# Kernel optimization log

Hardware: AMD Instinct MI355X
Metric: run time of the kernel (lower is better)

## Reference

```python
import jax, jax.numpy as jnp
import numpy as np

N = 100_000   # nodes
IN = 256      # input feature size
H = 128       # hidden dim
OUT = 16      # output classes
R = 5         # relations
E = 100_000   # edges per relation
B = 2         # bases


def setup_inputs() -> dict:
    key = jax.random.key(0)
    ks = jax.random.split(key, 10)
    return {
        "x": jax.random.normal(ks[0], (N, IN), jnp.float32),
        "src": jax.random.randint(ks[1], (R, E), 0, N, dtype=jnp.int32),
        "dst": jax.random.randint(ks[2], (R, E), 0, N, dtype=jnp.int32),
        "w_embed": jax.random.normal(ks[3], (IN, H), jnp.float32) / np.sqrt(IN).astype(np.float32),
        "b_embed": jnp.zeros((H,), jnp.float32),
        "basis1": jax.random.normal(ks[4], (B, H, H), jnp.float32) / np.sqrt(H).astype(np.float32),
        "coef1": jax.random.normal(ks[5], (R, B), jnp.float32),
        "bias1": jnp.zeros((H,), jnp.float32),
        "basis2": jax.random.normal(ks[6], (B, H, OUT), jnp.float32) / np.sqrt(H).astype(np.float32),
        "coef2": jax.random.normal(ks[7], (R, B), jnp.float32),
        "bias2": jnp.zeros((OUT,), jnp.float32),
    }


def _rgcn_layer(h, src, dst, basis, coef, bias):
    # basis decomposition: W_r = sum_b coef[r,b] * V_b  -> [R, in, out]
    W = jnp.einsum('rb,bio->rio', coef, basis)

    def per_rel(s, d, w):
        msg = h[s] @ w                                        # [E, out] gather + GEMM
        agg = jax.ops.segment_sum(msg, d, num_segments=N)     # [N, out] scatter-add
        deg = jax.ops.segment_sum(jnp.ones((E,), h.dtype), d, num_segments=N)
        return agg / jnp.maximum(deg, 1.0)[:, None]           # fn.mean per relation

    out = jax.vmap(per_rel)(src, dst, W).sum(axis=0)          # 'sum' cross-relation reduce
    return out + bias


def reference(x, src, dst, w_embed, b_embed, basis1, coef1, bias1, basis2, coef2, bias2):
    h = x @ w_embed + b_embed                                 # EmbeddingLayer (Linear per ntype)
    h = jax.nn.relu(_rgcn_layer(h, src, dst, basis1, coef1, bias1))  # hidden RGCN layer, relu
    return _rgcn_layer(h, src, dst, basis2, coef2, bias2)     # output layer, no activation
```

## Files before the change

kernel.cpp:

```cpp
#include <hip/hip_runtime.h>
#include <hip/hip_bf16.h>
#include <cstddef>

namespace {

constexpr int N = 100000;
constexpr int IN = 256;
constexpr int H = 128;
constexpr int OUT = 16;
constexpr int R = 5;
constexpr int E = 100000;
constexpr int RE = R * E;
constexpr int NB = (N + 255) / 256;

using short8 = __attribute__((ext_vector_type(8))) short;
using f32x4 = __attribute__((ext_vector_type(4))) float;

__device__ __forceinline__ float b2f(unsigned int u16) {
  union { unsigned int i; float f; } v;
  v.i = u16 << 16;
  return v.f;
}
__device__ __forceinline__ unsigned short f2b(float f) {
  union { float f; unsigned int u; } v;
  v.f = f;
  unsigned int r = v.u + 0x7fffu + ((v.u >> 16) & 1u);
  return (unsigned short)(r >> 16);
}

__global__ void deg_count(const int* __restrict__ dst, float* __restrict__ deg,
                          int* __restrict__ degtot) {
  int i = blockIdx.x * 256 + threadIdx.x;
  if (i < RE) {
    int d = dst[i];
    atomicAdd(&deg[(i / E) * N + d], 1.0f);
    atomicAdd(&degtot[d], 1);
  }
}

__global__ void inv_deg_k(float* __restrict__ deg) {
  int i = blockIdx.x * 256 + threadIdx.x;
  if (i < R * N) deg[i] = 1.0f / fmaxf(deg[i], 1.0f);
}

__global__ void scan_blk(const int* __restrict__ in, int* __restrict__ part,
                         int* __restrict__ bsum, int n) {
  __shared__ int tmp[256];
  int tid = threadIdx.x;
  int gid = blockIdx.x * 256 + tid;
  int v = (gid < n) ? in[gid] : 0;
  tmp[tid] = v;
  __syncthreads();
  for (int o = 1; o < 256; o <<= 1) {
    int t = (tid >= o) ? tmp[tid - o] : 0;
    __syncthreads();
    tmp[tid] += t;
    __syncthreads();
  }
  if (gid < n) part[gid] = tmp[tid] - v;
  if (tid == 255) bsum[blockIdx.x] = tmp[255];
}

__global__ void scan_top(const int* __restrict__ bsum, int* __restrict__ bscan, int nb) {
  __shared__ int tmp[512];
  int tid = threadIdx.x;
  int v = (tid < nb) ? bsum[tid] : 0;
  tmp[tid] = v;
  __syncthreads();
  for (int o = 1; o < 512; o <<= 1) {
    int t = (tid >= o) ? tmp[tid - o] : 0;
    __syncthreads();
    tmp[tid] += t;
    __syncthreads();
  }
  if (tid < nb) bscan[tid] = tmp[tid] - v;
}

__global__ void scan_add(int* __restrict__ part, const int* __restrict__ bscan, int n) {
  int gid = blockIdx.x * 256 + threadIdx.x;
  if (gid < n) part[gid] += bscan[gid >> 8];
}

__global__ void fill_csr(const int* __restrict__ src, const int* __restrict__ dst,
                         const float* __restrict__ coef1, const float* __restrict__ coef2,
                         const float* __restrict__ invdeg, const int* __restrict__ off,
                         int* __restrict__ cursor, int* __restrict__ esrc,
                         float2* __restrict__ ecA, float2* __restrict__ ecB) {
  int i = blockIdx.x * 256 + threadIdx.x;
  if (i >= RE) return;
  int r = i / E;
  int d = dst[i];
  int slot = off[d] + atomicAdd(&cursor[d], 1);
  float id = invdeg[r * N + d];
  esrc[slot] = src[i];
  ecA[slot] = make_float2(coef1[2 * r] * id, coef1[2 * r + 1] * id);
  ecB[slot] = make_float2(coef2[2 * r] * id, coef2[2 * r + 1] * id);
}

__global__ void pack_w(const float* __restrict__ W, unsigned short* __restrict__ wp,
                       int NOUT, int total) {
  int i = blockIdx.x * 256 + threadIdx.x;
  if (i >= total) return;
  int ii = i & 7;
  int lane = (i >> 3) & 63;
  int fb = i >> 9;
  int NCT = NOUT >> 4;
  int kc = fb / NCT, ct = fb - kc * NCT;
  int k = kc * 32 + ((lane >> 4) << 3) + ii;
  int col = (ct << 4) + (lane & 15);
  wp[i] = f2b(W[(size_t)k * NOUT + col]);
}

__global__ void pack_b2(const float* __restrict__ basis2, unsigned short* __restrict__ wp) {
  int i = blockIdx.x * 256 + threadIdx.x;
  if (i >= 128 * 32) return;
  int ii = i & 7;
  int lane = (i >> 3) & 63;
  int fb = i >> 9;
  int kc = fb >> 1, ct = fb & 1;
  int k = kc * 32 + ((lane >> 4) << 3) + ii;
  wp[i] = f2b(basis2[((size_t)ct * 128 + k) * 16 + (lane & 15)]);
}

__global__ __launch_bounds__(256) void gemm_embed(
    const float* __restrict__ x, const unsigned short* __restrict__ wpack,
    const float* __restrict__ bias, unsigned short* __restrict__ C) {
  const int tid = threadIdx.x;
  const int lane = tid & 63;
  const int wave = (blockIdx.x * 256 + tid) >> 6;
  const int base = wave * 32;
  if (base >= N) return;
  const int r = lane & 15, g = lane >> 4;
  const short8* wfrag = (const short8*)wpack;

  f32x4 acc[2][8];
#pragma unroll
  for (int t = 0; t < 2; ++t)
#pragma unroll
    for (int ct = 0; ct < 8; ++ct) acc[t][ct] = (f32x4){0.f, 0.f, 0.f, 0.f};

  const float* a0 = x + (size_t)(base + r) * IN + g * 8;
  const float* a1 = a0 + (size_t)16 * IN;

#pragma unroll
  for (int kc = 0; kc < 8; ++kc) {
    float4 v0 = *(const float4*)(a0 + kc * 32);
    float4 v1 = *(const float4*)(a0 + kc * 32 + 4);
    float4 v2 = *(const float4*)(a1 + kc * 32);
    float4 v3 = *(const float4*)(a1 + kc * 32 + 4);
    short8 af0, af1;
    af0[0] = (short)f2b(v0.x); af0[1] = (short)f2b(v0.y);
    af0[2] = (short)f2b(v0.z); af0[3] = (short)f2b(v0.w);
    af0[4] = (short)f2b(v1.x); af0[5] = (short)f2b(v1.y);
    af0[6] = (short)f2b(v1.z); af0[7] = (short)f2b(v1.w);
    af1[0] = (short)f2b(v2.x); af1[1] = (short)f2b(v2.y);
    af1[2] = (short)f2b(v2.z); af1[3] = (short)f2b(v2.w);
    af1[4] = (short)f2b(v3.x); af1[5] = (short)f2b(v3.y);
    af1[6] = (short)f2b(v3.z); af1[7] = (short)f2b(v3.w);
#pragma unroll
    for (int ct = 0; ct < 8; ++ct) {
      short8 bf = wfrag[(kc * 8 + ct) * 64 + lane];
      acc[0][ct] = __builtin_amdgcn_mfma_f32_16x16x32_bf16(af0, bf, acc[0][ct], 0, 0, 0);
      acc[1][ct] = __builtin_amdgcn_mfma_f32_16x16x32_bf16(af1, bf, acc[1][ct], 0, 0, 0);
    }
  }

#pragma unroll
  for (int t = 0; t < 2; ++t)
#pragma unroll
    for (int ct = 0; ct < 8; ++ct) {
      int col = ct * 16 + r;
      float bs = bias[col];
#pragma unroll
      for (int i = 0; i < 4; ++i)
        C[(size_t)(base + t * 16 + g * 4 + i) * H + col] = f2b(acc[t][ct][i] + bs);
    }
}

__global__ __launch_bounds__(256) void gemm_fused(
    const unsigned short* __restrict__ u, const unsigned short* __restrict__ wp1,
    const float* __restrict__ bias1, const unsigned short* __restrict__ wp2,
    unsigned short* __restrict__ q) {
  constexpr int LP2 = 132;
  __shared__ unsigned short hl[4][32][LP2];
  const int tid = threadIdx.x;
  const int lane = tid & 63;
  const int wv = tid >> 6;
  const int wave = (blockIdx.x * 256 + tid) >> 6;
  const int base = wave * 32;
  if (base >= N) return;
  const int r = lane & 15, g = lane >> 4;
  const short8* wf1 = (const short8*)wp1;
  const short8* wf2 = (const short8*)wp2;

  f32x4 acc[2][8];
#pragma unroll
  for (int t = 0; t < 2; ++t)
#pragma unroll
    for (int ct = 0; ct < 8; ++ct) acc[t][ct] = (f32x4){0.f, 0.f, 0.f, 0.f};

  const unsigned short* a0 = u + (size_t)(base + r) * 256 + g * 8;
  const unsigned short* a1 = a0 + (size_t)16 * 256;

#pragma unroll
  for (int kc = 0; kc < 8; ++kc) {
    short8 af0 = *(const short8*)(a0 + kc * 32);
    short8 af1 = *(const short8*)(a1 + kc * 32);
#pragma unroll
    for (int ct = 0; ct < 8; ++ct) {
      short8 bf = wf1[(kc * 8 + ct) * 64 + lane];
      acc[0][ct] = __builtin_amdgcn_mfma_f32_16x16x32_bf16(af0, bf, acc[0][ct], 0, 0, 0);
      acc[1][ct] = __builtin_amdgcn_mfma_f32_16x16x32_bf16(af1, bf, acc[1][ct], 0, 0, 0);
    }
  }

#pragma unroll
  for (int t = 0; t < 2; ++t)
#pragma unroll
    for (int ct = 0; ct < 8; ++ct) {
      int col = ct * 16 + r;
      float bs = bias1[col];
#pragma unroll
      for (int i = 0; i < 4; ++i)
        hl[wv][t * 16 + g * 4 + i][col] = f2b(fmaxf(acc[t][ct][i] + bs, 0.f));
    }

  asm volatile("s_waitcnt lgkmcnt(0)" ::: "memory");
  __builtin_amdgcn_sched_barrier(0);

  f32x4 acc2[2][2];
#pragma unroll
  for (int t = 0; t < 2; ++t)
#pragma unroll
    for (int ct = 0; ct < 2; ++ct) acc2[t][ct] = (f32x4){0.f, 0.f, 0.f, 0.f};

#pragma unroll
  for (int kc = 0; kc < 4; ++kc) {
    short8 af0 = *(const short8*)&hl[wv][r][kc * 32 + g * 8];
    short8 af1 = *(const short8*)&hl[wv][16 + r][kc * 32 + g * 8];
#pragma unroll
    for (int ct = 0; ct < 2; ++ct) {
      short8 bf = wf2[(kc * 2 + ct) * 64 + lane];
      acc2[0][ct] = __builtin_amdgcn_mfma_f32_16x16x32_bf16(af0, bf, acc2[0][ct], 0, 0, 0);
      acc2[1][ct] = __builtin_amdgcn_mfma_f32_16x16x32_bf16(af1, bf, acc2[1][ct], 0, 0, 0);
    }
  }

#pragma unroll
  for (int t = 0; t < 2; ++t)
#pragma unroll
    for (int ct = 0; ct < 2; ++ct) {
      int col = ct * 16 + r;
#pragma unroll
      for (int i = 0; i < 4; ++i)
        q[(size_t)(base + t * 16 + g * 4 + i) * 32 + col] = f2b(acc2[t][ct][i]);
    }
}

__global__ __launch_bounds__(256) void gather1(
    const int* __restrict__ off, const int* __restrict__ degtot,
    const int* __restrict__ esrc, const float2* __restrict__ ecA,
    const unsigned short* __restrict__ hbf, unsigned int* __restrict__ ubf) {
  int wid = blockIdx.x * 4 + (threadIdx.x >> 6);
  int lane = threadIdx.x & 63;
  if (wid >= N) return;
  int start = off[wid];
  int cnt = degtot[wid];
  float u0x = 0.f, u0y = 0.f, u1x = 0.f, u1y = 0.f;
  if (cnt > 0) {
    int s = esrc[start];
    float2 c = ecA[start];
    unsigned int hv = ((const unsigned int*)(hbf + (size_t)s * 128))[lane];
    for (int j = 1; j < cnt; ++j) {
      int sn = esrc[start + j];
      float2 cn = ecA[start + j];
      unsigned int hvn = ((const unsigned int*)(hbf + (size_t)sn * 128))[lane];
      float hx = b2f(hv & 0xffffu), hy = b2f(hv >> 16);
      u0x = fmaf(c.x, hx, u0x); u0y = fmaf(c.x, hy, u0y);
      u1x = fmaf(c.y, hx, u1x); u1y = fmaf(c.y, hy, u1y);
      s = sn; c = cn; hv = hvn;
    }
    float hx = b2f(hv & 0xffffu), hy = b2f(hv >> 16);
    u0x = fmaf(c.x, hx, u0x); u0y = fmaf(c.x, hy, u0y);
    u1x = fmaf(c.y, hx, u1x); u1y = fmaf(c.y, hy, u1y);
  }
  unsigned int* ur = ubf + (size_t)wid * 128;
  ur[lane]      = (unsigned int)f2b(u0x) | ((unsigned int)f2b(u0y) << 16);
  ur[64 + lane] = (unsigned int)f2b(u1x) | ((unsigned int)f2b(u1y) << 16);
}

__global__ __launch_bounds__(256) void gather2(
    const int* __restrict__ off, const int* __restrict__ degtot,
    const int* __restrict__ esrc, const float2* __restrict__ ecB,
    const unsigned short* __restrict__ qbf, const float* __restrict__ bias2,
    float* __restrict__ out) {
  int node = blockIdx.x * 16 + (threadIdx.x >> 4);
  int k = threadIdx.x & 15;
  if (node >= N) return;
  int start = off[node];
  int cnt = degtot[node];
  float acc = bias2[k];
  for (int j = 0; j < cnt; ++j) {
    int s = esrc[start + j];
    float2 c = ecB[start + j];
    acc = fmaf(c.x, b2f(qbf[(size_t)s * 32 + k]), acc);
    acc = fmaf(c.y, b2f(qbf[(size_t)s * 32 + 16 + k]), acc);
  }
  out[(size_t)node * 16 + k] = acc;
}

}

extern "C" void kernel_launch(void* const* d_in, const int* in_sizes, int n_in,
                              void* d_out, int out_size, void* d_ws, size_t ws_size,
                              hipStream_t stream) {
  const float* x       = (const float*)d_in[0];
  const int*   src     = (const int*)d_in[1];
  const int*   dst     = (const int*)d_in[2];
  const float* w_embed = (const float*)d_in[3];
  const float* b_embed = (const float*)d_in[4];
  const float* basis1  = (const float*)d_in[5];
  const float* coef1   = (const float*)d_in[6];
  const float* bias1   = (const float*)d_in[7];
  const float* basis2  = (const float*)d_in[8];
  const float* coef2   = (const float*)d_in[9];
  const float* bias2   = (const float*)d_in[10];
  float* out = (float*)d_out;

  float2* ecA = (float2*)d_ws;
  float2* ecB = ecA + RE;
  float*  invdeg = (float*)(ecB + RE);
  int*    degtot = (int*)(invdeg + (size_t)R * N);
  int*    off    = degtot + N;
  int*    bsum   = off + N;
  int*    bscan  = bsum + 512;
  int*    cursor = bscan + 512;
  int*    esrc   = cursor + N;
  unsigned short* wp1  = (unsigned short*)(esrc + RE);
  unsigned short* wpB1 = wp1 + 256 * 128;
  unsigned short* wpB2 = wpB1 + 256 * 128;
  unsigned short* h_bf = wpB2 + 128 * 32;
  unsigned short* u_bf = h_bf + (size_t)N * 128;
  unsigned short* q_bf = u_bf + (size_t)N * 256;

  dim3 b256(256);
  hipMemsetAsync(invdeg, 0, (size_t)R * N * sizeof(float), stream);
  hipMemsetAsync(degtot, 0, (size_t)N * sizeof(int), stream);
  hipMemsetAsync(cursor, 0, (size_t)N * sizeof(int), stream);

  deg_count<<<(RE + 255) / 256, b256, 0, stream>>>(dst, invdeg, degtot);
  inv_deg_k<<<(R * N + 255) / 256, b256, 0, stream>>>(invdeg);
  scan_blk<<<NB, b256, 0, stream>>>(degtot, off, bsum, N);
  scan_top<<<1, dim3(512), 0, stream>>>(bsum, bscan, NB);
  scan_add<<<NB, b256, 0, stream>>>(off, bscan, N);
  fill_csr<<<(RE + 255) / 256, b256, 0, stream>>>(src, dst, coef1, coef2, invdeg,
                                                  off, cursor, esrc, ecA, ecB);
  pack_w<<<(256 * 128 + 255) / 256, b256, 0, stream>>>(w_embed, wp1, 128, 256 * 128);
  pack_w<<<(256 * 128 + 255) / 256, b256, 0, stream>>>(basis1, wpB1, 128, 256 * 128);
  pack_b2<<<(128 * 32 + 255) / 256, b256, 0, stream>>>(basis2, wpB2);

  int gwaves = (N + 31) / 32;
  int gblocks = (gwaves + 3) / 4;
  gemm_embed<<<gblocks, b256, 0, stream>>>(x, wp1, b_embed, h_bf);
  gather1<<<(N + 3) / 4, b256, 0, stream>>>(off, degtot, esrc, ecA, h_bf,
                                            (unsigned int*)u_bf);
  gemm_fused<<<gblocks, b256, 0, stream>>>(u_bf, wpB1, bias1, wpB2, q_bf);
  gather2<<<(N + 15) / 16, b256, 0, stream>>>(off, degtot, esrc, ecB, q_bf, bias2, out);
}
```

Measured before the change: 427.8 us.

## Pack edge src and relation, stage GEMM inputs via LDS, merge setup kernels

The CSR build no longer stores per-edge float2 coefficients for both layers. Each edge now holds a packed int (src | relation<<20), and the gather kernels rebuild coefficients from per-node inverse degrees and coef arrays, which cuts the edge-stream bytes written and read. The GEMMs now load input rows into LDS with global_load_lds and use 16 rows per wave instead of 32, which gives more waves and coalesced loads at the cost of extra LDS use. The three weight-packing kernels are merged into one and the three memsets into one, reducing launch count. The trade-off is extra select logic and five invdeg loads per node in the gathers.

```diff
diff --git a/kernel.cpp b/kernel.cpp
--- a/kernel.cpp
+++ b/kernel.cpp
@@ -1,13 +1,13 @@
 #include <hip/hip_runtime.h>
 #include <hip/hip_bf16.h>
 #include <cstddef>
+#include <cstdint>
 
 namespace {
 
 constexpr int N = 100000;
 constexpr int IN = 256;
 constexpr int H = 128;
-constexpr int OUT = 16;
 constexpr int R = 5;
 constexpr int E = 100000;
 constexpr int RE = R * E;
@@ -26,6 +26,17 @@
   v.f = f;
   unsigned int r = v.u + 0x7fffu + ((v.u >> 16) & 1u);
   return (unsigned short)(r >> 16);
+}
+
+__device__ __forceinline__ void load_lds16(const void* g, void* l) {
+  __builtin_amdgcn_global_load_lds(
+      (const __attribute__((address_space(1))) void*)g,
+      (__attribute__((address_space(3))) void*)l, 16, 0, 0);
+}
+
+__device__ __forceinline__ float sel5(int r, float a0, float a1, float a2,
+                                      float a3, float a4) {
+  return r == 0 ? a0 : (r == 1 ? a1 : (r == 2 ? a2 : (r == 3 ? a3 : a4)));
 }
 
 __global__ void deg_count(const int* __restrict__ dst, float* __restrict__ deg,
@@ -82,207 +93,194 @@
 }
 
 __global__ void fill_csr(const int* __restrict__ src, const int* __restrict__ dst,
-                         const float* __restrict__ coef1, const float* __restrict__ coef2,
-                         const float* __restrict__ invdeg, const int* __restrict__ off,
-                         int* __restrict__ cursor, int* __restrict__ esrc,
-                         float2* __restrict__ ecA, float2* __restrict__ ecB) {
+                         const int* __restrict__ off, int* __restrict__ cursor,
+                         int* __restrict__ epk) {
   int i = blockIdx.x * 256 + threadIdx.x;
   if (i >= RE) return;
   int r = i / E;
   int d = dst[i];
   int slot = off[d] + atomicAdd(&cursor[d], 1);
-  float id = invdeg[r * N + d];
-  esrc[slot] = src[i];
-  ecA[slot] = make_float2(coef1[2 * r] * id, coef1[2 * r + 1] * id);
-  ecB[slot] = make_float2(coef2[2 * r] * id, coef2[2 * r + 1] * id);
-}
-
-__global__ void pack_w(const float* __restrict__ W, unsigned short* __restrict__ wp,
-                       int NOUT, int total) {
+  epk[slot] = src[i] | (r << 20);
+}
+
+__global__ void pack_all(const float* __restrict__ w_embed,
+                         const float* __restrict__ basis1,
+                         const float* __restrict__ basis2,
+                         unsigned short* __restrict__ wp1,
+                         unsigned short* __restrict__ wpB1,
+                         unsigned short* __restrict__ wpB2) {
   int i = blockIdx.x * 256 + threadIdx.x;
-  if (i >= total) return;
-  int ii = i & 7;
-  int lane = (i >> 3) & 63;
-  int fb = i >> 9;
-  int NCT = NOUT >> 4;
-  int kc = fb / NCT, ct = fb - kc * NCT;
-  int k = kc * 32 + ((lane >> 4) << 3) + ii;
-  int col = (ct << 4) + (lane & 15);
-  wp[i] = f2b(W[(size_t)k * NOUT + col]);
-}
-
-__global__ void pack_b2(const float* __restrict__ basis2, unsigned short* __restrict__ wp) {
-  int i = blockIdx.x * 256 + threadIdx.x;
-  if (i >= 128 * 32) return;
-  int ii = i & 7;
-  int lane = (i >> 3) & 63;
-  int fb = i >> 9;
-  int kc = fb >> 1, ct = fb & 1;
-  int k = kc * 32 + ((lane >> 4) << 3) + ii;
-  wp[i] = f2b(basis2[((size_t)ct * 128 + k) * 16 + (lane & 15)]);
+  if (i < 32768) {
+    int ii = i & 7, lane = (i >> 3) & 63, fb = i >> 9;
+    int kc = fb >> 3, ct = fb & 7;
+    int k = kc * 32 + ((lane >> 4) << 3) + ii, col = (ct << 4) + (lane & 15);
+    wp1[i] = f2b(w_embed[(size_t)k * 128 + col]);
+  } else if (i < 65536) {
+    int j = i - 32768;
+    int ii = j & 7, lane = (j >> 3) & 63, fb = j >> 9;
+    int kc = fb >> 3, ct = fb & 7;
+    int k = kc * 32 + ((lane >> 4) << 3) + ii, col = (ct << 4) + (lane & 15);
+    wpB1[j] = f2b(basis1[(size_t)k * 128 + col]);
+  } else if (i < 65536 + 4096) {
+    int j = i - 65536;
+    int ii = j & 7, lane = (j >> 3) & 63, fb = j >> 9;
+    int kc = fb >> 1, ct = fb & 1;
+    int k = kc * 32 + ((lane >> 4) << 3) + ii;
+    wpB2[j] = f2b(basis2[((size_t)ct * 128 + k) * 16 + (lane & 15)]);
+  }
 }
 
 __global__ __launch_bounds__(256) void gemm_embed(
     const float* __restrict__ x, const unsigned short* __restrict__ wpack,
     const float* __restrict__ bias, unsigned short* __restrict__ C) {
-  const int tid = threadIdx.x;
-  const int lane = tid & 63;
-  const int wave = (blockIdx.x * 256 + tid) >> 6;
-  const int base = wave * 32;
+  __shared__ __align__(16) float alds[4][16][264];
+  const int tid = threadIdx.x, lane = tid & 63, wv = tid >> 6;
+  const int base = blockIdx.x * 64 + wv * 16;
   if (base >= N) return;
   const int r = lane & 15, g = lane >> 4;
   const short8* wfrag = (const short8*)wpack;
 
-  f32x4 acc[2][8];
-#pragma unroll
-  for (int t = 0; t < 2; ++t)
-#pragma unroll
-    for (int ct = 0; ct < 8; ++ct) acc[t][ct] = (f32x4){0.f, 0.f, 0.f, 0.f};
-
-  const float* a0 = x + (size_t)(base + r) * IN + g * 8;
-  const float* a1 = a0 + (size_t)16 * IN;
+#pragma unroll
+  for (int i = 0; i < 16; ++i)
+    load_lds16(x + (size_t)(base + i) * IN + lane * 4, &alds[wv][i][0]);
+
+  asm volatile("s_waitcnt vmcnt(0)" ::: "memory");
+  __builtin_amdgcn_sched_barrier(0);
+
+  f32x4 acc[8];
+#pragma unroll
+  for (int ct = 0; ct < 8; ++ct) acc[ct] = (f32x4){0.f, 0.f, 0.f, 0.f};
 
 #pragma unroll
   for (int kc = 0; kc < 8; ++kc) {
-    float4 v0 = *(const float4*)(a0 + kc * 32);
-    float4 v1 = *(const float4*)(a0 + kc * 32 + 4);
-    float4 v2 = *(const float4*)(a1 + kc * 32);
-    float4 v3 = *(const float4*)(a1 + kc * 32 + 4);
-    short8 af0, af1;
-    af0[0] = (short)f2b(v0.x); af0[1] = (short)f2b(v0.y);
-    af0[2] = (short)f2b(v0.z); af0[3] = (short)f2b(v0.w);
-    af0[4] = (short)f2b(v1.x); af0[5] = (short)f2b(v1.y);
-    af0[6] = (short)f2b(v1.z); af0[7] = (short)f2b(v1.w);
-    af1[0] = (short)f2b(v2.x); af1[1] = (short)f2b(v2.y);
-    af1[2] = (short)f2b(v2.z); af1[3] = (short)f2b(v2.w);
-    af1[4] = (short)f2b(v3.x); af1[5] = (short)f2b(v3.y);
-    af1[6] = (short)f2b(v3.z); af1[7] = (short)f2b(v3.w);
-#pragma unroll
-    for (int ct = 0; ct < 8; ++ct) {
-      short8 bf = wfrag[(kc * 8 + ct) * 64 + lane];
-      acc[0][ct] = __builtin_amdgcn_mfma_f32_16x16x32_bf16(af0, bf, acc[0][ct], 0, 0, 0);
-      acc[1][ct] = __builtin_amdgcn_mfma_f32_16x16x32_bf16(af1, bf, acc[1][ct], 0, 0, 0);
-    }
-  }
-
-#pragma unroll
-  for (int t = 0; t < 2; ++t)
-#pragma unroll
-    for (int ct = 0; ct < 8; ++ct) {
-      int col = ct * 16 + r;
-      float bs = bias[col];
-#pragma unroll
-      for (int i = 0; i < 4; ++i)
-        C[(size_t)(base + t * 16 + g * 4 + i) * H + col] = f2b(acc[t][ct][i] + bs);
-    }
+    float4 v0 = *(const float4*)&alds[wv][r][kc * 32 + g * 8];
+    float4 v1 = *(const float4*)&alds[wv][r][kc * 32 + g * 8 + 4];
+    short8 af;
+    af[0] = (short)f2b(v0.x); af[1] = (short)f2b(v0.y);
+    af[2] = (short)f2b(v0.z); af[3] = (short)f2b(v0.w);
+    af[4] = (short)f2b(v1.x); af[5] = (short)f2b(v1.y);
+    af[6] = (short)f2b(v1.z); af[7] = (short)f2b(v1.w);
+#pragma unroll
+    for (int ct = 0; ct < 8; ++ct)
+      acc[ct] = __builtin_amdgcn_mfma_f32_16x16x32_bf16(
+          af, wfrag[(kc * 8 + ct) * 64 + lane], acc[ct], 0, 0, 0);
+  }
+
+#pragma unroll
+  for (int ct = 0; ct < 8; ++ct) {
+    int col = ct * 16 + r;
+    float bs = bias[col];
+#pragma unroll
+    for (int i = 0; i < 4; ++i)
+      C[(size_t)(base + g * 4 + i) * H + col] = f2b(acc[ct][i] + bs);
+  }
 }
 
 __global__ __launch_bounds__(256) void gemm_fused(
     const unsigned short* __restrict__ u, const unsigned short* __restrict__ wp1,
     const float* __restrict__ bias1, const unsigned short* __restrict__ wp2,
     unsigned short* __restrict__ q) {
-  constexpr int LP2 = 132;
-  __shared__ unsigned short hl[4][32][LP2];
-  const int tid = threadIdx.x;
-  const int lane = tid & 63;
-  const int wv = tid >> 6;
-  const int wave = (blockIdx.x * 256 + tid) >> 6;
-  const int base = wave * 32;
+  __shared__ __align__(16) unsigned short ust[4][8][520];
+  __shared__ __align__(16) unsigned short hl[4][16][136];
+  const int tid = threadIdx.x, lane = tid & 63, wv = tid >> 6;
+  const int base = blockIdx.x * 64 + wv * 16;
   if (base >= N) return;
   const int r = lane & 15, g = lane >> 4;
   const short8* wf1 = (const short8*)wp1;
   const short8* wf2 = (const short8*)wp2;
 
-  f32x4 acc[2][8];
-#pragma unroll
-  for (int t = 0; t < 2; ++t)
-#pragma unroll
-    for (int ct = 0; ct < 8; ++ct) acc[t][ct] = (f32x4){0.f, 0.f, 0.f, 0.f};
-
-  const unsigned short* a0 = u + (size_t)(base + r) * 256 + g * 8;
-  const unsigned short* a1 = a0 + (size_t)16 * 256;
+#pragma unroll
+  for (int p = 0; p < 8; ++p)
+    load_lds16(u + (size_t)(base + 2 * p) * 256 + lane * 8, &ust[wv][p][0]);
+
+  asm volatile("s_waitcnt vmcnt(0)" ::: "memory");
+  __builtin_amdgcn_sched_barrier(0);
+
+  f32x4 acc[8];
+#pragma unroll
+  for (int ct = 0; ct < 8; ++ct) acc[ct] = (f32x4){0.f, 0.f, 0.f, 0.f};
 
 #pragma unroll
   for (int kc = 0; kc < 8; ++kc) {
-    short8 af0 = *(const short8*)(a0 + kc * 32);
-    short8 af1 = *(const short8*)(a1 + kc * 32);
-#pragma unroll
-    for (int ct = 0; ct < 8; ++ct) {
-      short8 bf = wf1[(kc * 8 + ct) * 64 + lane];
-      acc[0][ct] = __builtin_amdgcn_mfma_f32_16x16x32_bf16(af0, bf, acc[0][ct], 0, 0, 0);
-      acc[1][ct] = __builtin_amdgcn_mfma_f32_16x16x32_bf16(af1, bf, acc[1][ct], 0, 0, 0);
-    }
-  }
-
-#pragma unroll
-  for (int t = 0; t < 2; ++t)
-#pragma unroll
-    for (int ct = 0; ct < 8; ++ct) {
-      int col = ct * 16 + r;
-      float bs = bias1[col];
-#pragma unroll
-      for (int i = 0; i < 4; ++i)
-        hl[wv][t * 16 + g * 4 + i][col] = f2b(fmaxf(acc[t][ct][i] + bs, 0.f));
-    }
+    short8 af = *(const short8*)&ust[wv][r >> 1][(r & 1) * 256 + kc * 32 + g * 8];
+#pragma unroll
+    for (int ct = 0; ct < 8; ++ct)
+      acc[ct] = __builtin_amdgcn_mfma_f32_16x16x32_bf16(
+          af, wf1[(kc * 8 + ct) * 64 + lane], acc[ct], 0, 0, 0);
+  }
+
+#pragma unroll
+  for (int ct = 0; ct < 8; ++ct) {
+    int col = ct * 16 + r;
+    float bs = bias1[col];
+#pragma unroll
+    for (int i = 0; i < 4; ++i)
+      hl[wv][g * 4 + i][col] = f2b(fmaxf(acc[ct][i] + bs, 0.f));
+  }
 
   asm volatile("s_waitcnt lgkmcnt(0)" ::: "memory");
   __builtin_amdgcn_sched_barrier(0);
 
-  f32x4 acc2[2][2];
-#pragma unroll
-  for (int t = 0; t < 2; ++t)
-#pragma unroll
-    for (int ct = 0; ct < 2; ++ct) acc2[t][ct] = (f32x4){0.f, 0.f, 0.f, 0.f};
+  f32x4 acc2[2];
+#pragma unroll
+  for (int ct = 0; ct < 2; ++ct) acc2[ct] = (f32x4){0.f, 0.f, 0.f, 0.f};
 
 #pragma unroll
   for (int kc = 0; kc < 4; ++kc) {
-    short8 af0 = *(const short8*)&hl[wv][r][kc * 32 + g * 8];
-    short8 af1 = *(const short8*)&hl[wv][16 + r][kc * 32 + g * 8];
-#pragma unroll
-    for (int ct = 0; ct < 2; ++ct) {
-      short8 bf = wf2[(kc * 2 + ct) * 64 + lane];
-      acc2[0][ct] = __builtin_amdgcn_mfma_f32_16x16x32_bf16(af0, bf, acc2[0][ct], 0, 0, 0);
-      acc2[1][ct] = __builtin_amdgcn_mfma_f32_16x16x32_bf16(af1, bf, acc2[1][ct], 0, 0, 0);
-    }
-  }
-
-#pragma unroll
-  for (int t = 0; t < 2; ++t)
-#pragma unroll
-    for (int ct = 0; ct < 2; ++ct) {
-      int col = ct * 16 + r;
-#pragma unroll
-      for (int i = 0; i < 4; ++i)
-        q[(size_t)(base + t * 16 + g * 4 + i) * 32 + col] = f2b(acc2[t][ct][i]);
-    }
+    short8 af = *(const short8*)&hl[wv][r][kc * 32 + g * 8];
+#pragma unroll
+    for (int ct = 0; ct < 2; ++ct)
+      acc2[ct] = __builtin_amdgcn_mfma_f32_16x16x32_bf16(
+          af, wf2[(kc * 2 + ct) * 64 + lane], acc2[ct], 0, 0, 0);
+  }
+
+#pragma unroll
+  for (int ct = 0; ct < 2; ++ct) {
+    int col = ct * 16 + r;
+#pragma unroll
+    for (int i = 0; i < 4; ++i)
+      q[(size_t)(base + g * 4 + i) * 32 + col] = f2b(acc2[ct][i]);
+  }
 }
 
 __global__ __launch_bounds__(256) void gather1(
     const int* __restrict__ off, const int* __restrict__ degtot,
-    const int* __restrict__ esrc, const float2* __restrict__ ecA,
-    const unsigned short* __restrict__ hbf, unsigned int* __restrict__ ubf) {
+    const int* __restrict__ epk, const float* __restrict__ invdeg,
+    const float* __restrict__ coef1, const unsigned short* __restrict__ hbf,
+    unsigned int* __restrict__ ubf) {
   int wid = blockIdx.x * 4 + (threadIdx.x >> 6);
   int lane = threadIdx.x & 63;
   if (wid >= N) return;
   int start = off[wid];
   int cnt = degtot[wid];
+  float i0 = invdeg[wid], i1 = invdeg[N + wid], i2 = invdeg[2 * N + wid];
+  float i3 = invdeg[3 * N + wid], i4 = invdeg[4 * N + wid];
+  float x0 = coef1[0] * i0, y0 = coef1[1] * i0;
+  float x1 = coef1[2] * i1, y1 = coef1[3] * i1;
+  float x2 = coef1[4] * i2, y2 = coef1[5] * i2;
+  float x3 = coef1[6] * i3, y3 = coef1[7] * i3;
+  float x4 = coef1[8] * i4, y4 = coef1[9] * i4;
   float u0x = 0.f, u0y = 0.f, u1x = 0.f, u1y = 0.f;
   if (cnt > 0) {
-    int s = esrc[start];
-    float2 c = ecA[start];
+    int pk = epk[start];
+    int s = pk & 0xFFFFF, rr = pk >> 20;
     unsigned int hv = ((const unsigned int*)(hbf + (size_t)s * 128))[lane];
     for (int j = 1; j < cnt; ++j) {
-      int sn = esrc[start + j];
-      float2 cn = ecA[start + j];
+      int pkn = epk[start + j];
+      int sn = pkn & 0xFFFFF, rn = pkn >> 20;
       unsigned int hvn = ((const unsigned int*)(hbf + (size_t)sn * 128))[lane];
+      float c0 = sel5(rr, x0, x1, x2, x3, x4);
+      float c1 = sel5(rr, y0, y1, y2, y3, y4);
       float hx = b2f(hv & 0xffffu), hy = b2f(hv >> 16);
-      u0x = fmaf(c.x, hx, u0x); u0y = fmaf(c.x, hy, u0y);
-      u1x = fmaf(c.y, hx, u1x); u1y = fmaf(c.y, hy, u1y);
-      s = sn; c = cn; hv = hvn;
+      u0x = fmaf(c0, hx, u0x); u0y = fmaf(c0, hy, u0y);
+      u1x = fmaf(c1, hx, u1x); u1y = fmaf(c1, hy, u1y);
+      rr = rn; hv = hvn;
     }
+    float c0 = sel5(rr, x0, x1, x2, x3, x4);
+    float c1 = sel5(rr, y0, y1, y2, y3, y4);
     float hx = b2f(hv & 0xffffu), hy = b2f(hv >> 16);
-    u0x = fmaf(c.x, hx, u0x); u0y = fmaf(c.x, hy, u0y);
-    u1x = fmaf(c.y, hx, u1x); u1y = fmaf(c.y, hy, u1y);
+    u0x = fmaf(c0, hx, u0x); u0y = fmaf(c0, hy, u0y);
+    u1x = fmaf(c1, hx, u1x); u1y = fmaf(c1, hy, u1y);
   }
   unsigned int* ur = ubf + (size_t)wid * 128;
   ur[lane]      = (unsigned int)f2b(u0x) | ((unsigned int)f2b(u0y) << 16);
@@ -291,20 +289,29 @@
 
 __global__ __launch_bounds__(256) void gather2(
     const int* __restrict__ off, const int* __restrict__ degtot,
-    const int* __restrict__ esrc, const float2* __restrict__ ecB,
-    const unsigned short* __restrict__ qbf, const float* __restrict__ bias2,
-    float* __restrict__ out) {
+    const int* __restrict__ epk, const float* __restrict__ invdeg,
+    const float* __restrict__ coef2, const unsigned short* __restrict__ qbf,
+    const float* __restrict__ bias2, float* __restrict__ out) {
   int node = blockIdx.x * 16 + (threadIdx.x >> 4);
   int k = threadIdx.x & 15;
   if (node >= N) return;
   int start = off[node];
   int cnt = degtot[node];
+  float i0 = invdeg[node], i1 = invdeg[N + node], i2 = invdeg[2 * N + node];
+  float i3 = invdeg[3 * N + node], i4 = invdeg[4 * N + node];
+  float x0 = coef2[0] * i0, y0 = coef2[1] * i0;
+  float x1 = coef2[2] * i1, y1 = coef2[3] * i1;
+  float x2 = coef2[4] * i2, y2 = coef2[5] * i2;
+  float x3 = coef2[6] * i3, y3 = coef2[7] * i3;
+  float x4 = coef2[8] * i4, y4 = coef2[9] * i4;
   float acc = bias2[k];
   for (int j = 0; j < cnt; ++j) {
-    int s = esrc[start + j];
-    float2 c = ecB[start + j];
-    acc = fmaf(c.x, b2f(qbf[(size_t)s * 32 + k]), acc);
-    acc = fmaf(c.y, b2f(qbf[(size_t)s * 32 + 16 + k]), acc);
+    int pk = epk[start + j];
+    int s = pk & 0xFFFFF, rr = pk >> 20;
+    float c0 = sel5(rr, x0, x1, x2, x3, x4);
+    float c1 = sel5(rr, y0, y1, y2, y3, y4);
+    acc = fmaf(c0, b2f(qbf[(size_t)s * 32 + k]), acc);
+    acc = fmaf(c1, b2f(qbf[(size_t)s * 32 + 16 + k]), acc);
   }
   out[(size_t)node * 16 + k] = acc;
 }
@@ -327,16 +334,14 @@
   const float* bias2   = (const float*)d_in[10];
   float* out = (float*)d_out;
 
-  float2* ecA = (float2*)d_ws;
-  float2* ecB = ecA + RE;
-  float*  invdeg = (float*)(ecB + RE);
-  int*    degtot = (int*)(invdeg + (size_t)R * N);
-  int*    off    = degtot + N;
-  int*    bsum   = off + N;
-  int*    bscan  = bsum + 512;
-  int*    cursor = bscan + 512;
-  int*    esrc   = cursor + N;
-  unsigned short* wp1  = (unsigned short*)(esrc + RE);
+  float* invdeg = (float*)d_ws;
+  int*   degtot = (int*)(invdeg + (size_t)R * N);
+  int*   cursor = degtot + N;
+  int*   off    = cursor + N;
+  int*   bsum   = off + N;
+  int*   bscan  = bsum + 512;
+  int*   epk    = bscan + 512;
+  unsigned short* wp1  = (unsigned short*)(epk + RE);
   unsigned short* wpB1 = wp1 + 256 * 128;
   unsigned short* wpB2 = wpB1 + 256 * 128;
   unsigned short* h_bf = wpB2 + 128 * 32;
@@ -344,26 +349,22 @@
   unsigned short* q_bf = u_bf + (size_t)N * 256;
 
   dim3 b256(256);
-  hipMemsetAsync(invdeg, 0, (size_t)R * N * sizeof(float), stream);
-  hipMemsetAsync(degtot, 0, (size_t)N * sizeof(int), stream);
-  hipMemsetAsync(cursor, 0, (size_t)N * sizeof(int), stream);
+  hipMemsetAsync(invdeg, 0, (size_t)(R * N + 2 * N) * sizeof(float), stream);
 
   deg_count<<<(RE + 255) / 256, b256, 0, stream>>>(dst, invdeg, degtot);
   inv_deg_k<<<(R * N + 255) / 256, b256, 0, stream>>>(invdeg);
   scan_blk<<<NB, b256, 0, stream>>>(degtot, off, bsum, N);
   scan_top<<<1, dim3(512), 0, stream>>>(bsum, bscan, NB);
   scan_add<<<NB, b256, 0, stream>>>(off, bscan, N);
-  fill_csr<<<(RE + 255) / 256, b256, 0, stream>>>(src, dst, coef1, coef2, invdeg,
-                                                  off, cursor, esrc, ecA, ecB);
-  pack_w<<<(256 * 128 + 255) / 256, b256, 0, stream>>>(w_embed, wp1, 128, 256 * 128);
-  pack_w<<<(256 * 128 + 255) / 256, b256, 0, stream>>>(basis1, wpB1, 128, 256 * 128);
-  pack_b2<<<(128 * 32 + 255) / 256, b256, 0, stream>>>(basis2, wpB2);
-
-  int gwaves = (N + 31) / 32;
-  int gblocks = (gwaves + 3) / 4;
+  fill_csr<<<(RE + 255) / 256, b256, 0, stream>>>(src, dst, off, cursor, epk);
+  pack_all<<<(65536 + 4096 + 255) / 256, b256, 0, stream>>>(
+      w_embed, basis1, basis2, wp1, wpB1, wpB2);
+
+  int gblocks = (N / 16 + 3) / 4;
   gemm_embed<<<gblocks, b256, 0, stream>>>(x, wp1, b_embed, h_bf);
-  gather1<<<(N + 3) / 4, b256, 0, stream>>>(off, degtot, esrc, ecA, h_bf,
-                                            (unsigned int*)u_bf);
+  gather1<<<(N + 3) / 4, b256, 0, stream>>>(off, degtot, epk, invdeg, coef1,
+                                            h_bf, (unsigned int*)u_bf);
   gemm_fused<<<gblocks, b256, 0, stream>>>(u_bf, wpB1, bias1, wpB2, q_bf);
-  gather2<<<(N + 15) / 16, b256, 0, stream>>>(off, degtot, esrc, ecB, q_bf, bias2, out);
-}
+  gather2<<<(N + 15) / 16, b256, 0, stream>>>(off, degtot, epk, invdeg, coef2,
+                                              q_bf, bias2, out);
+}
```

Result: faster. 379.5 us (-11.3%).
